# Optimization experiments

Hardware: AMD Instinct MI355X
Metric: run time of the kernel (lower is better)

The kernel has to match this reference:

```python
import jax, jax.numpy as jnp
import numpy as np

N, D, C, S, E, K, MIN_MATCH, N_ITER = 100000, 128, 16, 16, 3200000, 64, 1, 4


def setup_inputs() -> dict:
    key = jax.random.key(0)
    k1, k2, k3, k4 = jax.random.split(key, 4)
    es = jax.random.normal(k1, (N, D), jnp.float32)
    edge_index = jax.random.randint(k2, (2, E), 0, N)
    seeds = jax.random.randint(k3, (C, S), 0, N)
    W = jax.random.normal(k4, (D, D), jnp.float32) / np.float32(np.sqrt(D))
    return {"es": es, "edge_index": edge_index, "seeds": seeds, "W": W, "n_iter": N_ITER}


def _memory_step(es, idx, hx, W):
    # ragged gather of last expansion, padded to fixed size per class: [C, k, D]
    inp = es[idx]
    d = inp.shape[-1]
    q = jnp.mean(inp, axis=1) if hx is None else hx          # attention query [C, D]
    logits = jnp.einsum('ckd,cd->ck', inp, q) / jnp.sqrt(jnp.float32(d))
    a = jax.nn.softmax(logits, axis=-1)                      # [C, k]
    ctx = jnp.einsum('ck,ckd->cd', a, inp)                   # attended read [C, D]
    pre = ctx if hx is None else ctx + hx                    # recurrent memory update
    return jnp.tanh(pre @ W)                                 # [C, D]


def _cosine(x, y):
    xn = x / (jnp.linalg.norm(x, axis=-1, keepdims=True) + 1e-8)
    yn = y / (jnp.linalg.norm(y, axis=-1, keepdims=True) + 1e-8)
    return xn @ yn.T                                         # [N, C]


def _expand(es, W, edge_index, seeds, n_iter):
    n, c = es.shape[0], seeds.shape[0]
    src, dst = edge_index[0], edge_index[1]
    # known_mask.scatter_(0, seed_all, 1)
    known = jnp.zeros((n,), bool).at[seeds.ravel()].set(True)
    # get_cate_mask(seeds, N): per-class membership mask [C, N]
    cate = jnp.zeros((c, n), bool).at[jnp.arange(c)[:, None], seeds].set(True)
    hx, last = None, seeds
    outs, exps, hxes = [], [], []
    for _ in range(n_iter):
        hx = _memory_step(es, last, hx, W)
        # get_cate_neighbors: per-class count of in-edges whose source is in the class
        counts = jax.vmap(lambda m: jax.ops.segment_sum(m, dst, num_segments=n))(
            cate.astype(jnp.float32)[:, src])                # [C, N]
        valid = (counts >= MIN_MATCH) & (~known)[None, :]    # [C, N]
        scores = _cosine(es, hx).T                           # [C, N]
        # _select: top n_expansion valid nodes per class (finite fill avoids -inf grads)
        probs, idx = jax.lax.top_k(jnp.where(valid, scores, -1e9), K)
        known = known.at[idx.ravel()].set(True)
        cate = cate.at[jnp.arange(c)[:, None], idx].set(True)
        last = idx
        outs.append(probs); exps.append(idx); hxes.append(hx)
    return jnp.stack(outs), jnp.stack(exps), jnp.stack(hxes)


def reference(es, edge_index, seeds, W, n_iter):
    return _expand(es, W, edge_index, seeds, n_iter)
```

## Files before the change

### kernel.cpp

```cpp
#include <hip/hip_runtime.h>
#include <math.h>

#define NN 100000
#define DD 128
#define CC 16
#define SS 16
#define EE 3200000
#define KK 64
#define NIT 4
#define CNT_STRIDE 32
#define NB 32
#define SLMAX 4096
#define MM (NB * KK)
#define EBLK 2048
#define INF_STAMP 0x7fffffff

typedef unsigned long long ull;

__device__ inline ull ordkey(double d) {
    long long b = __double_as_longlong(d);
    return (b < 0) ? ~(ull)b : ((ull)b | 0x8000000000000000ULL);
}
__device__ inline double keyord(ull u) {
    long long b = (u & 0x8000000000000000ULL)
                    ? (long long)(u & 0x7FFFFFFFFFFFFFFFULL)
                    : (long long)~u;
    return __longlong_as_double(b);
}
__device__ inline bool gt(ull ka, int na, ull kb, int nb) {
    return (ka > kb) || (ka == kb && na < nb);
}

__device__ inline void wsort64(ull& k, int& n, int lane) {
    for (int k2 = 2; k2 <= 64; k2 <<= 1) {
        for (int j = k2 >> 1; j; j >>= 1) {
            ull ok = __shfl_xor(k, j, 64);
            int on = __shfl_xor(n, j, 64);
            bool isLow = (lane & j) == 0;
            bool d = (k2 == 64) || ((lane & k2) == 0);
            bool wantMax = (d == isLow);
            if (wantMax == gt(ok, on, k, n)) { k = ok; n = on; }
        }
    }
}
__device__ inline void wmerge64(ull& k, int& n, int lane) {
    for (int j = 32; j; j >>= 1) {
        ull ok = __shfl_xor(k, j, 64);
        int on = __shfl_xor(n, j, 64);
        bool wantMax = (lane & j) == 0;
        if (wantMax == gt(ok, on, k, n)) { k = ok; n = on; }
    }
}


__global__ __launch_bounds__(256)
void k_init(const int* __restrict__ seeds, int* __restrict__ known,
            unsigned* __restrict__ cate, unsigned* __restrict__ nbr) {
    __shared__ int sd[CC * SS];
    int tid = threadIdx.x;
    if (tid < CC * SS) sd[tid] = seeds[tid];
    __syncthreads();
    int wave = tid >> 6, lane = tid & 63;
    int n = blockIdx.x * 4 + wave;
    if (n >= NN) return;
    unsigned m = 0;
    #pragma unroll
    for (int e = lane; e < CC * SS; e += 64)
        if (sd[e] == n) m |= 1u << (e / SS);
    for (int o = 32; o > 0; o >>= 1) m |= __shfl_xor(m, o, 64);
    if (lane == 0) {
        known[n] = m ? 0 : INF_STAMP;
        cate[n] = m;
        nbr[n] = 0;
    }
}


__global__ __launch_bounds__(256)
void k_memedge(const float* __restrict__ es, const float* __restrict__ Wm,
               const int* __restrict__ seeds, const int* __restrict__ last,
               double* __restrict__ hx, double* __restrict__ hxn,
               float* __restrict__ out, int* __restrict__ cnt,
               const int* __restrict__ edge, const unsigned* __restrict__ cate,
               unsigned* __restrict__ nbr, int t) {
    __shared__ float  inp[KK][DD + 1];
    __shared__ int    rowS[KK];
    __shared__ double q[DD];
    __shared__ double lg[KK];
    __shared__ double sr[KK];
    __shared__ double pre[DD];
    __shared__ double red[DD];
    int tid = threadIdx.x;

    if (blockIdx.x >= CC) {
        for (long e = (long)(blockIdx.x - CC) * 256 + tid; e < EE;
             e += (long)EBLK * 256) {
            int s = edge[e];
            unsigned m = cate[s];
            if (m) atomicOr(&nbr[edge[EE + e]], m);
        }
        return;
    }

    int c = blockIdx.x;
    if (tid == 0) cnt[c * CNT_STRIDE] = 0;
    int k = (t == 0) ? SS : KK;
    if (tid < KK) {
        lg[tid] = -1.0e308;
        if (tid < k) rowS[tid] = (t == 0) ? seeds[c * SS + tid] : last[c * KK + tid];
    }
    __syncthreads();
    for (int i = tid; i < k * DD; i += 256)
        inp[i >> 7][i & 127] = es[(long)rowS[i >> 7] * DD + (i & 127)];
    __syncthreads();
    if (tid < DD) {
        if (t == 0) {
            double s = 0;
            for (int j = 0; j < k; ++j) s += (double)inp[j][tid];
            q[tid] = s / (double)k;
        } else {
            q[tid] = hx[c * DD + tid];
        }
    }
    __syncthreads();
    if (tid < k) {
        double s = 0;
        for (int i = 0; i < DD; ++i) s += (double)inp[tid][i] * q[i];
        lg[tid] = s / sqrt((double)DD);
    }
    __syncthreads();
    if (tid < KK) sr[tid] = lg[tid];
    __syncthreads();
    for (int st = 32; st > 0; st >>= 1) {
        if (tid < st) sr[tid] = fmax(sr[tid], sr[tid + st]);
        __syncthreads();
    }
    double mx = sr[0];
    __syncthreads();
    if (tid < KK) {
        double e = (tid < k) ? exp(lg[tid] - mx) : 0.0;
        lg[tid] = e; sr[tid] = e;
    }
    __syncthreads();
    for (int st = 32; st > 0; st >>= 1) {
        if (tid < st) sr[tid] += sr[tid + st];
        __syncthreads();
    }
    double sm = sr[0];
    __syncthreads();
    if (tid < KK) lg[tid] /= sm;
    __syncthreads();
    if (tid < DD) {
        double ctx = 0;
        for (int j = 0; j < k; ++j) ctx += lg[j] * (double)inp[j][tid];
        pre[tid] = (t == 0) ? ctx : (ctx + q[tid]);
    }
    __syncthreads();
    double h = 0;
    if (tid < DD) {
        for (int i = 0; i < DD; ++i) h += pre[i] * (double)Wm[i * DD + tid];
        h = tanh(h);
        red[tid] = h * h;
    }
    __syncthreads();
    for (int st = 64; st > 0; st >>= 1) {
        if (tid < st) red[tid] += red[tid + st];
        __syncthreads();
    }
    if (tid < DD) {
        double inv = 1.0 / (sqrt(red[0]) + 1e-8);
        hx[c * DD + tid] = h;
        hxn[c * DD + tid] = h * inv;
        out[2 * NIT * CC * KK + t * CC * DD + c * DD + tid] = (float)h;
    }
}


__global__ __launch_bounds__(256)
void k_cand(const float* __restrict__ es,
            const int* __restrict__ known, const unsigned* __restrict__ nbr,
            const double* __restrict__ hxn,
            int* __restrict__ cnt, int* __restrict__ cidx,
            ull* __restrict__ ckey, int cap, int t) {
    __shared__ int    pair[256 * 16];
    __shared__ short  prank[256 * 16];
    __shared__ double hxnL[CC * 129];
    __shared__ int    lcnt[CC];
    __shared__ int    base[CC];
    __shared__ int    npair;
    int tid = threadIdx.x;

    for (int i = tid; i < CC * DD; i += 256)
        hxnL[(i >> 7) * 129 + (i & 127)] = hxn[i];
    if (tid < CC) lcnt[tid] = 0;
    if (tid == 0) npair = 0;
    __syncthreads();

    int n = blockIdx.x * 256 + tid;
    unsigned m = 0;
    if (n < NN && known[n] > t) m = nbr[n];
    while (m) {
        int c = __ffs(m) - 1;
        m &= m - 1;
        int r = atomicAdd(&lcnt[c], 1);
        int p = atomicAdd(&npair, 1);
        pair[p] = (n << 4) | c;
        prank[p] = (short)r;
    }
    __syncthreads();

    if (tid < CC && lcnt[tid] > 0)
        base[tid] = atomicAdd(&cnt[tid * CNT_STRIDE], lcnt[tid]);
    __syncthreads();

    int np = npair;
    for (int t2 = tid; t2 < np; t2 += 256) {
        int pk = pair[t2];
        int nn = pk >> 4, c = pk & 15;
        const float4* row = (const float4*)(es + (long)nn * DD);
        const double* h = &hxnL[c * 129];
        double s = 0, p2 = 0;
        #pragma unroll
        for (int i = 0; i < 32; ++i) {
            float4 v = row[i];
            double vx = v.x, vy = v.y, vz = v.z, vw = v.w;
            s  += vx * h[4 * i + 0] + vy * h[4 * i + 1]
                + vz * h[4 * i + 2] + vw * h[4 * i + 3];
            p2 += vx * vx + vy * vy + vz * vz + vw * vw;
        }
        int pos = base[c] + (int)prank[t2];
        if (pos < cap) {
            cidx[(long)c * cap + pos] = nn;
            ckey[(long)c * cap + pos] = ordkey(s / (sqrt(p2) + 1e-8));
        }
    }
}


__global__ __launch_bounds__(256)
void k_top(const int* __restrict__ cnt, const int* __restrict__ cidx,
           const ull* __restrict__ ckey, int cap,
           ull* __restrict__ tkey, int* __restrict__ tnode) {
    __shared__ ull ks[SLMAX];
    __shared__ int ns[SLMAX];
    int c = blockIdx.x / NB, b = blockIdx.x % NB;
    int tid = threadIdx.x, wave = tid >> 6, lane = tid & 63;
    int count = min(cnt[c * CNT_STRIDE], cap);
    int per = (count + NB - 1) / NB;
    int start = b * per;
    int m = min(per, count - start);
    int sl = 64;
    while (sl < per) sl <<= 1;
    int nruns = sl >> 6;
    for (int r = wave; r < nruns; r += 4) {
        int i = (r << 6) + lane;
        ull k; int n;
        if (i < m) { k = ckey[(long)c * cap + start + i]; n = cidx[(long)c * cap + start + i]; }
        else       { k = 0ULL; n = 0x7FFFFFFF; }
        wsort64(k, n, lane);
        ks[i] = k; ns[i] = n;
    }
    __syncthreads();
    for (int step = 1; step < nruns; step <<= 1) {
        int npair2 = nruns / (2 * step);
        for (int pr = wave; pr < npair2; pr += 4) {
            int ra = pr * 2 * step, rb = ra + step;
            ull ka = ks[(ra << 6) + lane];       int na = ns[(ra << 6) + lane];
            ull kb = ks[(rb << 6) + 63 - lane];  int nb2 = ns[(rb << 6) + 63 - lane];
            if (gt(kb, nb2, ka, na)) { ka = kb; na = nb2; }
            wmerge64(ka, na, lane);
            ks[(ra << 6) + lane] = ka; ns[(ra << 6) + lane] = na;
        }
        __syncthreads();
    }
    if (tid < KK) {
        tkey[(long)c * MM + b * KK + tid] = ks[tid];
        tnode[(long)c * MM + b * KK + tid] = ns[tid];
    }
}


__global__ __launch_bounds__(256)
void k_mergeupd(const int* __restrict__ cnt,
                const ull* __restrict__ tkey, const int* __restrict__ tnode,
                int* __restrict__ known, const unsigned* __restrict__ nbr,
                unsigned* __restrict__ cate, int* __restrict__ last,
                float* __restrict__ out, int cap, int t) {
    __shared__ ull ks[MM];
    __shared__ int ns[MM];
    int c = blockIdx.x, tid = threadIdx.x, wave = tid >> 6, lane = tid & 63;
    for (int i = tid; i < MM; i += 256) {
        ks[i] = tkey[(long)c * MM + i];
        ns[i] = tnode[(long)c * MM + i];
    }
    __syncthreads();
    for (int step = 1; step < NB; step <<= 1) {
        int npair2 = NB / (2 * step);
        for (int pr = wave; pr < npair2; pr += 4) {
            int ra = pr * 2 * step, rb = ra + step;
            ull ka = ks[(ra << 6) + lane];       int na = ns[(ra << 6) + lane];
            ull kb = ks[(rb << 6) + 63 - lane];  int nb2 = ns[(rb << 6) + 63 - lane];
            if (gt(kb, nb2, ka, na)) { ka = kb; na = nb2; }
            wmerge64(ka, na, lane);
            ks[(ra << 6) + lane] = ka; ns[(ra << 6) + lane] = na;
        }
        __syncthreads();
    }
    int count = min(cnt[c * CNT_STRIDE], cap);
    int nsel = min(count, KK);
    if (tid < KK && tid < nsel) {
        int n = ns[tid];
        out[t * CC * KK + c * KK + tid] = (float)keyord(ks[tid]);
        out[NIT * CC * KK + t * CC * KK + c * KK + tid] = (float)n;
        last[c * KK + tid] = n;
        known[n] = t + 1;
        atomicOr(&cate[n], 1u << c);
    }
    if (tid == 0 && nsel < KK) {
        int r = nsel;
        for (int n = 0; n < NN && r < KK; ++n) {
            bool valid = ((nbr[n] >> c) & 1u) && (known[n] > t);
            if (!valid) {
                out[t * CC * KK + c * KK + r] = -1e9f;
                out[NIT * CC * KK + t * CC * KK + c * KK + r] = (float)n;
                last[c * KK + r] = n;
                known[n] = t + 1;
                atomicOr(&cate[n], 1u << c);
                ++r;
            }
        }
    }
}


extern "C" void kernel_launch(void* const* d_in, const int* in_sizes, int n_in,
                              void* d_out, int out_size, void* d_ws, size_t ws_size,
                              hipStream_t stream) {
    const float* es    = (const float*)d_in[0];
    const int*   edge  = (const int*)d_in[1];
    const int*   seeds = (const int*)d_in[2];
    const float* W     = (const float*)d_in[3];
    float* out = (float*)d_out;

    char* p = (char*)d_ws;
    auto alloc = [&](size_t bytes) -> char* {
        char* r = p;
        p += (bytes + 255) & ~(size_t)255;
        return r;
    };
    int*      known    = (int*)alloc((size_t)NN * 4);
    unsigned* cate     = (unsigned*)alloc((size_t)NN * 4);
    unsigned* nbr      = (unsigned*)alloc((size_t)NN * 4);
    double*   hx       = (double*)alloc(CC * DD * 8);
    double*   hxn      = (double*)alloc(CC * DD * 8);
    int*      last     = (int*)alloc(CC * KK * 4);
    int*      cnt      = (int*)alloc(CC * CNT_STRIDE * 4);
    ull*      tkey     = (ull*)alloc((size_t)CC * MM * 8);
    int*      tnode    = (int*)alloc((size_t)CC * MM * 4);
    size_t used = (size_t)(p - (char*)d_ws);
    size_t rem = (ws_size > used + 8192) ? (ws_size - used - 8192) : 0;
    long capl = (long)(rem / (CC * 12));
    if (capl > NN) capl = NN;
    if (capl < 1) capl = 1;
    int cap = (int)capl;
    int*    cidx = (int*)alloc((size_t)CC * cap * 4);
    ull*    ckey = (ull*)alloc((size_t)CC * cap * 8);

    k_init<<<(NN + 3) / 4, 256, 0, stream>>>(seeds, known, cate, nbr);

    for (int t = 0; t < NIT; ++t) {
        k_memedge<<<CC + EBLK, 256, 0, stream>>>(es, W, seeds, last, hx, hxn, out,
                                                 cnt, edge, cate, nbr, t);
        k_cand<<<(NN + 255) / 256, 256, 0, stream>>>(es, known, nbr, hxn,
                                                     cnt, cidx, ckey, cap, t);
        k_top<<<CC * NB, 256, 0, stream>>>(cnt, cidx, ckey, cap, tkey, tnode);
        k_mergeupd<<<CC, 256, 0, stream>>>(cnt, tkey, tnode, known, nbr,
                                           cate, last, out, cap, t);
    }
}
```

Baseline: 303.9 us.

## Fuse candidate scoring and per-block top-k into a single kernel

Merges the candidate-filtering/cosine-scoring kernel and the per-block top-k sort kernel into one. Each block now owns a fixed node range for one class, collects its valid candidates directly into shared memory, scores them and sorts them in place. This removes the global candidate index/key buffers, their write and re-read, the capacity logic and one kernel launch. In exchange, every class block rescans the known/nbr arrays for its range, and the fixed range size must stay within the shared sort buffer.

```diff
diff --git a/kernel.cpp b/kernel.cpp
--- a/kernel.cpp
+++ b/kernel.cpp
@@ -10,6 +10,7 @@
 #define NIT 4
 #define CNT_STRIDE 32
 #define NB 32
+#define PER ((NN + NB - 1) / NB)
 #define SLMAX 4096
 #define MM (NB * KK)
 #define EBLK 2048
@@ -177,88 +178,57 @@
 
 
 __global__ __launch_bounds__(256)
-void k_cand(const float* __restrict__ es,
-            const int* __restrict__ known, const unsigned* __restrict__ nbr,
-            const double* __restrict__ hxn,
-            int* __restrict__ cnt, int* __restrict__ cidx,
-            ull* __restrict__ ckey, int cap, int t) {
-    __shared__ int    pair[256 * 16];
-    __shared__ short  prank[256 * 16];
-    __shared__ double hxnL[CC * 129];
-    __shared__ int    lcnt[CC];
-    __shared__ int    base[CC];
-    __shared__ int    npair;
-    int tid = threadIdx.x;
-
-    for (int i = tid; i < CC * DD; i += 256)
-        hxnL[(i >> 7) * 129 + (i & 127)] = hxn[i];
-    if (tid < CC) lcnt[tid] = 0;
-    if (tid == 0) npair = 0;
-    __syncthreads();
-
-    int n = blockIdx.x * 256 + tid;
-    unsigned m = 0;
-    if (n < NN && known[n] > t) m = nbr[n];
-    while (m) {
-        int c = __ffs(m) - 1;
-        m &= m - 1;
-        int r = atomicAdd(&lcnt[c], 1);
-        int p = atomicAdd(&npair, 1);
-        pair[p] = (n << 4) | c;
-        prank[p] = (short)r;
-    }
-    __syncthreads();
-
-    if (tid < CC && lcnt[tid] > 0)
-        base[tid] = atomicAdd(&cnt[tid * CNT_STRIDE], lcnt[tid]);
-    __syncthreads();
-
-    int np = npair;
-    for (int t2 = tid; t2 < np; t2 += 256) {
-        int pk = pair[t2];
-        int nn = pk >> 4, c = pk & 15;
+void k_candtop(const float* __restrict__ es,
+               const int* __restrict__ known, const unsigned* __restrict__ nbr,
+               const double* __restrict__ hxn, int* __restrict__ cnt,
+               ull* __restrict__ tkey, int* __restrict__ tnode, int t) {
+    __shared__ ull ks[SLMAX];
+    __shared__ int ns[SLMAX];
+    __shared__ double hL[DD];
+    __shared__ int lcnt;
+    int c = blockIdx.x / NB, b = blockIdx.x % NB;
+    int tid = threadIdx.x, wave = tid >> 6, lane = tid & 63;
+
+    if (tid < DD) hL[tid] = hxn[c * DD + tid];
+    if (tid == 0) lcnt = 0;
+    __syncthreads();
+
+    int start = b * PER, end = min(start + PER, NN);
+    for (int n = start + tid; n < end; n += 256) {
+        if (known[n] > t && ((nbr[n] >> c) & 1u)) {
+            int r = atomicAdd(&lcnt, 1);
+            ns[r] = n;
+        }
+    }
+    __syncthreads();
+    int m = lcnt;
+    if (tid == 0 && m > 0) atomicAdd(&cnt[c * CNT_STRIDE], m);
+
+    for (int i = tid; i < m; i += 256) {
+        int nn = ns[i];
         const float4* row = (const float4*)(es + (long)nn * DD);
-        const double* h = &hxnL[c * 129];
         double s = 0, p2 = 0;
         #pragma unroll
-        for (int i = 0; i < 32; ++i) {
-            float4 v = row[i];
+        for (int j = 0; j < 32; ++j) {
+            float4 v = row[j];
             double vx = v.x, vy = v.y, vz = v.z, vw = v.w;
-            s  += vx * h[4 * i + 0] + vy * h[4 * i + 1]
-                + vz * h[4 * i + 2] + vw * h[4 * i + 3];
+            s  += vx * hL[4 * j + 0] + vy * hL[4 * j + 1]
+                + vz * hL[4 * j + 2] + vw * hL[4 * j + 3];
             p2 += vx * vx + vy * vy + vz * vz + vw * vw;
         }
-        int pos = base[c] + (int)prank[t2];
-        if (pos < cap) {
-            cidx[(long)c * cap + pos] = nn;
-            ckey[(long)c * cap + pos] = ordkey(s / (sqrt(p2) + 1e-8));
-        }
-    }
-}
-
-
-__global__ __launch_bounds__(256)
-void k_top(const int* __restrict__ cnt, const int* __restrict__ cidx,
-           const ull* __restrict__ ckey, int cap,
-           ull* __restrict__ tkey, int* __restrict__ tnode) {
-    __shared__ ull ks[SLMAX];
-    __shared__ int ns[SLMAX];
-    int c = blockIdx.x / NB, b = blockIdx.x % NB;
-    int tid = threadIdx.x, wave = tid >> 6, lane = tid & 63;
-    int count = min(cnt[c * CNT_STRIDE], cap);
-    int per = (count + NB - 1) / NB;
-    int start = b * per;
-    int m = min(per, count - start);
+        ks[i] = ordkey(s / (sqrt(p2) + 1e-8));
+    }
     int sl = 64;
-    while (sl < per) sl <<= 1;
+    while (sl < m) sl <<= 1;
     int nruns = sl >> 6;
+    for (int i = m + tid; i < sl; i += 256) { ks[i] = 0ULL; ns[i] = 0x7FFFFFFF; }
+    __syncthreads();
+
     for (int r = wave; r < nruns; r += 4) {
         int i = (r << 6) + lane;
-        ull k; int n;
-        if (i < m) { k = ckey[(long)c * cap + start + i]; n = cidx[(long)c * cap + start + i]; }
-        else       { k = 0ULL; n = 0x7FFFFFFF; }
-        wsort64(k, n, lane);
-        ks[i] = k; ns[i] = n;
+        ull k = ks[i]; int n2 = ns[i];
+        wsort64(k, n2, lane);
+        ks[i] = k; ns[i] = n2;
     }
     __syncthreads();
     for (int step = 1; step < nruns; step <<= 1) {
@@ -285,7 +255,7 @@
                 const ull* __restrict__ tkey, const int* __restrict__ tnode,
                 int* __restrict__ known, const unsigned* __restrict__ nbr,
                 unsigned* __restrict__ cate, int* __restrict__ last,
-                float* __restrict__ out, int cap, int t) {
+                float* __restrict__ out, int t) {
     __shared__ ull ks[MM];
     __shared__ int ns[MM];
     int c = blockIdx.x, tid = threadIdx.x, wave = tid >> 6, lane = tid & 63;
@@ -306,7 +276,7 @@
         }
         __syncthreads();
     }
-    int count = min(cnt[c * CNT_STRIDE], cap);
+    int count = cnt[c * CNT_STRIDE];
     int nsel = min(count, KK);
     if (tid < KK && tid < nsel) {
         int n = ns[tid];
@@ -357,24 +327,15 @@
     int*      cnt      = (int*)alloc(CC * CNT_STRIDE * 4);
     ull*      tkey     = (ull*)alloc((size_t)CC * MM * 8);
     int*      tnode    = (int*)alloc((size_t)CC * MM * 4);
-    size_t used = (size_t)(p - (char*)d_ws);
-    size_t rem = (ws_size > used + 8192) ? (ws_size - used - 8192) : 0;
-    long capl = (long)(rem / (CC * 12));
-    if (capl > NN) capl = NN;
-    if (capl < 1) capl = 1;
-    int cap = (int)capl;
-    int*    cidx = (int*)alloc((size_t)CC * cap * 4);
-    ull*    ckey = (ull*)alloc((size_t)CC * cap * 8);
 
     k_init<<<(NN + 3) / 4, 256, 0, stream>>>(seeds, known, cate, nbr);
 
     for (int t = 0; t < NIT; ++t) {
         k_memedge<<<CC + EBLK, 256, 0, stream>>>(es, W, seeds, last, hx, hxn, out,
                                                  cnt, edge, cate, nbr, t);
-        k_cand<<<(NN + 255) / 256, 256, 0, stream>>>(es, known, nbr, hxn,
-                                                     cnt, cidx, ckey, cap, t);
-        k_top<<<CC * NB, 256, 0, stream>>>(cnt, cidx, ckey, cap, tkey, tnode);
+        k_candtop<<<CC * NB, 256, 0, stream>>>(es, known, nbr, hxn, cnt,
+                                               tkey, tnode, t);
         k_mergeupd<<<CC, 256, 0, stream>>>(cnt, tkey, tnode, known, nbr,
-                                           cate, last, out, cap, t);
-    }
-}
+                                           cate, last, out, t);
+    }
+}
```

After: 334.2 us. 1.1x slower.

## Fuse per-chunk top-k and final merge via last-block-done counter

Applied to the files above, without the earlier changes.

Merges the k_top and k_mergeupd kernels into one launch. Each block publishes its partial top-64 with atomics, then bumps a per-class counter, and the last block to finish for a class does the final merge and update. This removes one kernel launch and its boundary per iteration. The cost is atomic stores and loads plus fences, and the final merge now runs on a single block per class at the tail of a larger kernel.

```diff
diff --git a/kernel.cpp b/kernel.cpp
--- a/kernel.cpp
+++ b/kernel.cpp
@@ -55,11 +55,13 @@
 
 __global__ __launch_bounds__(256)
 void k_init(const int* __restrict__ seeds, int* __restrict__ known,
-            unsigned* __restrict__ cate, unsigned* __restrict__ nbr) {
+            unsigned* __restrict__ cate, unsigned* __restrict__ nbr,
+            unsigned* __restrict__ done) {
     __shared__ int sd[CC * SS];
     int tid = threadIdx.x;
     if (tid < CC * SS) sd[tid] = seeds[tid];
     __syncthreads();
+    if (blockIdx.x == 0 && tid < CC) done[tid] = 0;
     int wave = tid >> 6, lane = tid & 63;
     int n = blockIdx.x * 4 + wave;
     if (n >= NN) return;
@@ -238,11 +240,16 @@
 
 
 __global__ __launch_bounds__(256)
-void k_top(const int* __restrict__ cnt, const int* __restrict__ cidx,
-           const ull* __restrict__ ckey, int cap,
-           ull* __restrict__ tkey, int* __restrict__ tnode) {
+void k_topmerge(const int* __restrict__ cnt, const int* __restrict__ cidx,
+                const ull* __restrict__ ckey, int cap,
+                ull* __restrict__ tkey, int* __restrict__ tnode,
+                unsigned* __restrict__ done,
+                int* __restrict__ known, const unsigned* __restrict__ nbr,
+                unsigned* __restrict__ cate, int* __restrict__ last,
+                float* __restrict__ out, int t) {
     __shared__ ull ks[SLMAX];
     __shared__ int ns[SLMAX];
+    __shared__ int iswin;
     int c = blockIdx.x / NB, b = blockIdx.x % NB;
     int tid = threadIdx.x, wave = tid >> 6, lane = tid & 63;
     int count = min(cnt[c * CNT_STRIDE], cap);
@@ -274,24 +281,23 @@
         __syncthreads();
     }
     if (tid < KK) {
-        tkey[(long)c * MM + b * KK + tid] = ks[tid];
-        tnode[(long)c * MM + b * KK + tid] = ns[tid];
-    }
-}
-
-
-__global__ __launch_bounds__(256)
-void k_mergeupd(const int* __restrict__ cnt,
-                const ull* __restrict__ tkey, const int* __restrict__ tnode,
-                int* __restrict__ known, const unsigned* __restrict__ nbr,
-                unsigned* __restrict__ cate, int* __restrict__ last,
-                float* __restrict__ out, int cap, int t) {
-    __shared__ ull ks[MM];
-    __shared__ int ns[MM];
-    int c = blockIdx.x, tid = threadIdx.x, wave = tid >> 6, lane = tid & 63;
+        atomicExch(&tkey[(long)c * MM + b * KK + tid], ks[tid]);
+        atomicExch((unsigned*)&tnode[(long)c * MM + b * KK + tid], (unsigned)ns[tid]);
+    }
+    __syncthreads();
+    if (tid == 0) {
+        __threadfence();
+        unsigned old = atomicAdd(&done[c], 1u);
+        iswin = (old == NB - 1);
+        if (iswin) atomicExch(&done[c], 0u);
+    }
+    __syncthreads();
+    if (!iswin) return;
+
+    __threadfence();
     for (int i = tid; i < MM; i += 256) {
-        ks[i] = tkey[(long)c * MM + i];
-        ns[i] = tnode[(long)c * MM + i];
+        ks[i] = atomicOr(&tkey[(long)c * MM + i], 0ULL);
+        ns[i] = (int)atomicOr((unsigned*)&tnode[(long)c * MM + i], 0u);
     }
     __syncthreads();
     for (int step = 1; step < NB; step <<= 1) {
@@ -306,7 +312,6 @@
         }
         __syncthreads();
     }
-    int count = min(cnt[c * CNT_STRIDE], cap);
     int nsel = min(count, KK);
     if (tid < KK && tid < nsel) {
         int n = ns[tid];
@@ -357,6 +362,7 @@
     int*      cnt      = (int*)alloc(CC * CNT_STRIDE * 4);
     ull*      tkey     = (ull*)alloc((size_t)CC * MM * 8);
     int*      tnode    = (int*)alloc((size_t)CC * MM * 4);
+    unsigned* done     = (unsigned*)alloc(CC * 4);
     size_t used = (size_t)(p - (char*)d_ws);
     size_t rem = (ws_size > used + 8192) ? (ws_size - used - 8192) : 0;
     long capl = (long)(rem / (CC * 12));
@@ -366,15 +372,14 @@
     int*    cidx = (int*)alloc((size_t)CC * cap * 4);
     ull*    ckey = (ull*)alloc((size_t)CC * cap * 8);
 
-    k_init<<<(NN + 3) / 4, 256, 0, stream>>>(seeds, known, cate, nbr);
+    k_init<<<(NN + 3) / 4, 256, 0, stream>>>(seeds, known, cate, nbr, done);
 
     for (int t = 0; t < NIT; ++t) {
         k_memedge<<<CC + EBLK, 256, 0, stream>>>(es, W, seeds, last, hx, hxn, out,
                                                  cnt, edge, cate, nbr, t);
         k_cand<<<(NN + 255) / 256, 256, 0, stream>>>(es, known, nbr, hxn,
                                                      cnt, cidx, ckey, cap, t);
-        k_top<<<CC * NB, 256, 0, stream>>>(cnt, cidx, ckey, cap, tkey, tnode);
-        k_mergeupd<<<CC, 256, 0, stream>>>(cnt, tkey, tnode, known, nbr,
-                                           cate, last, out, cap, t);
-    }
-}
+        k_topmerge<<<CC * NB, 256, 0, stream>>>(cnt, cidx, ckey, cap, tkey, tnode,
+                                                done, known, nbr, cate, last, out, t);
+    }
+}
```

New measurement: 358.4 us. 1.18x slower.

## Propagate neighbor masks incrementally from newly known sources and split FP64 accumulators

Applied to the files above, without the earlier changes.

The edge pass now only ORs class masks from sources whose known stamp equals the current iteration, i.e. nodes added in the last step. It relies on nbr accumulating across iterations instead of recomputing from every source with a nonzero class mask, which cuts the atomics and cate loads to a small set of edges. The dot-product loops in the memory step and in candidate scoring also use several independent double accumulators to break serial FMA dependency chains, which slightly changes summation order. Correctness depends on the stamp semantics of known being set consistently by the init and update kernels.

```diff
diff --git a/kernel.cpp b/kernel.cpp
--- a/kernel.cpp
+++ b/kernel.cpp
@@ -82,7 +82,7 @@
                double* __restrict__ hx, double* __restrict__ hxn,
                float* __restrict__ out, int* __restrict__ cnt,
                const int* __restrict__ edge, const unsigned* __restrict__ cate,
-               unsigned* __restrict__ nbr, int t) {
+               const int* __restrict__ known, unsigned* __restrict__ nbr, int t) {
     __shared__ float  inp[KK][DD + 1];
     __shared__ int    rowS[KK];
     __shared__ double q[DD];
@@ -96,8 +96,10 @@
         for (long e = (long)(blockIdx.x - CC) * 256 + tid; e < EE;
              e += (long)EBLK * 256) {
             int s = edge[e];
-            unsigned m = cate[s];
-            if (m) atomicOr(&nbr[edge[EE + e]], m);
+            if (known[s] == t) {
+                unsigned m = cate[s];
+                atomicOr(&nbr[edge[EE + e]], m);
+            }
         }
         return;
     }
@@ -124,9 +126,14 @@
     }
     __syncthreads();
     if (tid < k) {
-        double s = 0;
-        for (int i = 0; i < DD; ++i) s += (double)inp[tid][i] * q[i];
-        lg[tid] = s / sqrt((double)DD);
+        double s0 = 0, s1 = 0, s2 = 0, s3 = 0;
+        for (int i = 0; i < DD; i += 4) {
+            s0 += (double)inp[tid][i + 0] * q[i + 0];
+            s1 += (double)inp[tid][i + 1] * q[i + 1];
+            s2 += (double)inp[tid][i + 2] * q[i + 2];
+            s3 += (double)inp[tid][i + 3] * q[i + 3];
+        }
+        lg[tid] = ((s0 + s1) + (s2 + s3)) / sqrt((double)DD);
     }
     __syncthreads();
     if (tid < KK) sr[tid] = lg[tid];
@@ -151,15 +158,27 @@
     if (tid < KK) lg[tid] /= sm;
     __syncthreads();
     if (tid < DD) {
-        double ctx = 0;
-        for (int j = 0; j < k; ++j) ctx += lg[j] * (double)inp[j][tid];
+        double c0 = 0, c1 = 0, c2 = 0, c3 = 0;
+        for (int j = 0; j < k; j += 4) {
+            c0 += lg[j + 0] * (double)inp[j + 0][tid];
+            c1 += lg[j + 1] * (double)inp[j + 1][tid];
+            c2 += lg[j + 2] * (double)inp[j + 2][tid];
+            c3 += lg[j + 3] * (double)inp[j + 3][tid];
+        }
+        double ctx = (c0 + c1) + (c2 + c3);
         pre[tid] = (t == 0) ? ctx : (ctx + q[tid]);
     }
     __syncthreads();
     double h = 0;
     if (tid < DD) {
-        for (int i = 0; i < DD; ++i) h += pre[i] * (double)Wm[i * DD + tid];
-        h = tanh(h);
+        double h0 = 0, h1 = 0, h2 = 0, h3 = 0;
+        for (int i = 0; i < DD; i += 4) {
+            h0 += pre[i + 0] * (double)Wm[(i + 0) * DD + tid];
+            h1 += pre[i + 1] * (double)Wm[(i + 1) * DD + tid];
+            h2 += pre[i + 2] * (double)Wm[(i + 2) * DD + tid];
+            h3 += pre[i + 3] * (double)Wm[(i + 3) * DD + tid];
+        }
+        h = tanh((h0 + h1) + (h2 + h3));
         red[tid] = h * h;
     }
     __syncthreads();
@@ -219,15 +238,25 @@
         int nn = pk >> 4, c = pk & 15;
         const float4* row = (const float4*)(es + (long)nn * DD);
         const double* h = &hxnL[c * 129];
-        double s = 0, p2 = 0;
+        double sx0 = 0, sy0 = 0, sz0 = 0, sw0 = 0;
+        double sx1 = 0, sy1 = 0, sz1 = 0, sw1 = 0;
+        double px0 = 0, py0 = 0, pz0 = 0, pw0 = 0;
+        double px1 = 0, py1 = 0, pz1 = 0, pw1 = 0;
         #pragma unroll
-        for (int i = 0; i < 32; ++i) {
+        for (int i = 0; i < 32; i += 2) {
             float4 v = row[i];
+            float4 u = row[i + 1];
             double vx = v.x, vy = v.y, vz = v.z, vw = v.w;
-            s  += vx * h[4 * i + 0] + vy * h[4 * i + 1]
-                + vz * h[4 * i + 2] + vw * h[4 * i + 3];
-            p2 += vx * vx + vy * vy + vz * vz + vw * vw;
-        }
+            double ux = u.x, uy = u.y, uz = u.z, uw = u.w;
+            sx0 += vx * h[4 * i + 0];  sy0 += vy * h[4 * i + 1];
+            sz0 += vz * h[4 * i + 2];  sw0 += vw * h[4 * i + 3];
+            sx1 += ux * h[4 * i + 4];  sy1 += uy * h[4 * i + 5];
+            sz1 += uz * h[4 * i + 6];  sw1 += uw * h[4 * i + 7];
+            px0 += vx * vx;  py0 += vy * vy;  pz0 += vz * vz;  pw0 += vw * vw;
+            px1 += ux * ux;  py1 += uy * uy;  pz1 += uz * uz;  pw1 += uw * uw;
+        }
+        double s  = (((sx0 + sy0) + (sz0 + sw0)) + ((sx1 + sy1) + (sz1 + sw1)));
+        double p2 = (((px0 + py0) + (pz0 + pw0)) + ((px1 + py1) + (pz1 + pw1)));
         int pos = base[c] + (int)prank[t2];
         if (pos < cap) {
             cidx[(long)c * cap + pos] = nn;
@@ -370,7 +399,7 @@
 
     for (int t = 0; t < NIT; ++t) {
         k_memedge<<<CC + EBLK, 256, 0, stream>>>(es, W, seeds, last, hx, hxn, out,
-                                                 cnt, edge, cate, nbr, t);
+                                                 cnt, edge, cate, known, nbr, t);
         k_cand<<<(NN + 255) / 256, 256, 0, stream>>>(es, known, nbr, hxn,
                                                      cnt, cidx, ckey, cap, t);
         k_top<<<CC * NB, 256, 0, stream>>>(cnt, cidx, ckey, cap, tkey, tnode);
```

Measured after the change: 303.4 us, median of 2. No clear change (-0.2%).
